# Kernel tuning notes

Hardware: AMD Instinct MI355X
Metric: run time of the kernel (lower is better)

Reference implementation:

```python
import jax, jax.numpy as jnp
import numpy as np

N_NODES = 100000
N_EDGES = 1600000
IN_DIM = 128
HID = 128
OUT = 128
NUM_GRAPHS = 2048


def setup_inputs() -> dict:
    key = jax.random.key(0)
    ks = jax.random.split(key, 10)
    x = jax.random.normal(ks[0], (N_NODES, IN_DIM), dtype=jnp.float32)
    edge_index = jax.random.randint(ks[1], (2, N_EDGES), 0, N_NODES, dtype=jnp.int32)
    graph_index = jnp.sort(jax.random.randint(ks[2], (N_NODES,), 0, NUM_GRAPHS, dtype=jnp.int32))
    def glorot(k, fi, fo):
        lim = jnp.sqrt(6.0 / (fi + fo)).astype(jnp.float32)
        return jax.random.uniform(k, (fi, fo), jnp.float32, -lim, lim)
    return {
        "x": x,
        "edge_index": edge_index,
        "graph_index": graph_index,
        "num_graphs": NUM_GRAPHS,
        "W1": glorot(ks[3], IN_DIM, HID), "b1": jnp.zeros((HID,), jnp.float32),
        "W2": glorot(ks[4], HID, HID),    "b2": jnp.zeros((HID,), jnp.float32),
        "W3": glorot(ks[5], HID, OUT),    "b3": jnp.zeros((OUT,), jnp.float32),
    }


def _gcn_layer(x, src, dst, norm, W, b, n_nodes):
    # transform first (cheap GEMM), then normalized gather-scatter aggregation
    h = x @ W                              # [N, F]
    msg = h[src] * norm[:, None]           # [E+N, F] gather + scale
    out = jax.ops.segment_sum(msg, dst, num_segments=n_nodes)  # scatter-add
    return out + b


def reference(x, edge_index, graph_index, num_graphs, W1, b1, W2, b2, W3, b3):
    n = x.shape[0]
    # add self-loops (PyG GCNConv default)
    loops = jnp.arange(n, dtype=edge_index.dtype)
    src = jnp.concatenate([edge_index[0], loops])
    dst = jnp.concatenate([edge_index[1], loops])
    # symmetric normalization D^-1/2 (A+I) D^-1/2, degree = in-degree incl. self-loop
    deg = jax.ops.segment_sum(jnp.ones_like(src, dtype=x.dtype), dst, num_segments=n)
    dinv = jax.lax.rsqrt(jnp.maximum(deg, 1.0))
    norm = dinv[src] * dinv[dst]
    # 3 conv layers + ReLU (dropout = identity at inference)
    h = jax.nn.relu(_gcn_layer(x, src, dst, norm, W1, b1, n))
    h = jax.nn.relu(_gcn_layer(h, src, dst, norm, W2, b2, n))
    h = jax.nn.relu(_gcn_layer(h, src, dst, norm, W3, b3, n))
    # global mean / max pooling per graph
    gsum = jax.ops.segment_sum(h, graph_index, num_segments=num_graphs)
    cnt = jax.ops.segment_sum(jnp.ones((n,), h.dtype), graph_index, num_segments=num_graphs)
    gmean = gsum / jnp.maximum(cnt, 1.0)[:, None]
    gmax = jax.ops.segment_max(h, graph_index, num_segments=num_graphs)
    return jnp.concatenate([gmean, gmax], axis=-1)
```

## Files before the change

kernel.cpp:

```cpp
#include <hip/hip_runtime.h>
#include <hip/hip_bf16.h>
#include <stdint.h>

#define N_NODES   100000
#define N_EDGES   1600000
#define FDIM      128
#define NUM_GR    2048
#define CSR_CAP   64

#define NBKT      391
#define BKT_CAP   4864
#define TILE      2048
#define LBIN_CAP  24

typedef __attribute__((ext_vector_type(8))) short short8;
typedef __attribute__((ext_vector_type(4))) float f32x4;

__device__ __forceinline__ uint32_t pk2(float a, float b) {
    __hip_bfloat16 x = __float2bfloat16(a), y = __float2bfloat16(b);
    uint16_t ux = *reinterpret_cast<uint16_t*>(&x);
    uint16_t uy = *reinterpret_cast<uint16_t*>(&y);
    return (uint32_t)ux | ((uint32_t)uy << 16);
}

__device__ __forceinline__ float bflo(uint32_t u) { return __uint_as_float(u << 16); }
__device__ __forceinline__ float bfhi(uint32_t u) { return __uint_as_float(u & 0xFFFF0000u); }


__global__ __launch_bounds__(256) void k_bucket_wprep(
        const int* __restrict__ src, const int* __restrict__ dst,
        int* __restrict__ bkt_cnt, int* __restrict__ bkt, int E, int gA,
        const float* __restrict__ W1, const float* __restrict__ W2,
        const float* __restrict__ W3, __hip_bfloat16* __restrict__ wt) {
    int b = blockIdx.x;
    if (b >= gA) {
        int idx = (b - gA) * 256 + threadIdx.x;
        int l = idx >> 14, rem = idx & 16383, c = rem >> 7, k = rem & 127;
        const float* W = (l == 0) ? W1 : ((l == 1) ? W2 : W3);
        wt[idx] = __float2bfloat16(W[k * FDIM + c]);
        return;
    }

    __shared__ int binCnt[NBKT];
    __shared__ int binBase[NBKT];
    __shared__ int bins[NBKT * LBIN_CAP];

    for (int i = threadIdx.x; i < NBKT; i += 256) binCnt[i] = 0;
    __syncthreads();

    int e0 = b * TILE;
    int e1 = min(E, e0 + TILE);
    for (int e = e0 + threadIdx.x; e < e1; e += 256) {
        int s = src[e];
        int d = dst[e];
        int bi = d >> 8;
        int rec = ((d & 255) << 17) | s;
        int pos = atomicAdd(&binCnt[bi], 1);
        if (pos < LBIN_CAP) {
            bins[bi * LBIN_CAP + pos] = rec;
        } else {
            int gp = atomicAdd(&bkt_cnt[bi], 1);
            if (gp < BKT_CAP) bkt[bi * BKT_CAP + gp] = rec;
        }
    }
    __syncthreads();

    for (int i = threadIdx.x; i < NBKT; i += 256) {
        int c = min(binCnt[i], LBIN_CAP);
        binBase[i] = (c > 0) ? atomicAdd(&bkt_cnt[i], c) : 0;
    }
    __syncthreads();

    for (int i = threadIdx.x; i < NBKT * LBIN_CAP; i += 256) {
        int bi = i / LBIN_CAP, sl = i - bi * LBIN_CAP;
        if (sl < min(binCnt[bi], LBIN_CAP)) {
            int gp = binBase[bi] + sl;
            if (gp < BKT_CAP) bkt[bi * BKT_CAP + gp] = bins[i];
        }
    }
}


__global__ __launch_bounds__(256) void k_csr(const int* __restrict__ bkt_cnt,
                                             const int* __restrict__ bkt,
                                             int* __restrict__ cnt,
                                             float* __restrict__ dinv,
                                             int* __restrict__ csr, int n) {
    __shared__ int lc[256];
    __shared__ int cur[256];
    int b = blockIdx.x;
    int tid = threadIdx.x;
    lc[tid] = 0;
    cur[tid] = 0;
    __syncthreads();

    int len = min(bkt_cnt[b], BKT_CAP);
    const int* recs = bkt + b * BKT_CAP;

    for (int i = tid; i < len; i += 256)
        atomicAdd(&lc[(recs[i] >> 17) & 255], 1);
    __syncthreads();

    int v = (b << 8) + tid;
    if (v < n) {
        int c = lc[tid];
        cnt[v] = c;
        dinv[v] = rsqrtf((float)(c + 1));
    }

    for (int i = tid; i < len; i += 256) {
        int rec = recs[i];
        int dl = (rec >> 17) & 255;
        int pos = atomicAdd(&cur[dl], 1);
        if (pos < CSR_CAP)
            csr[(((size_t)(b << 8) + dl) << 6) + pos] = rec & 0x1FFFF;
    }
}


template<bool AF32>
__global__ __launch_bounds__(256) void k_gemm(const void* __restrict__ Ap,
                                              const __hip_bfloat16* __restrict__ Wt,
                                              const float* __restrict__ dinv,
                                              __hip_bfloat16* __restrict__ C, int n) {
    __shared__ uint32_t lds[2 * 128 * 64];
    uint32_t* Atl = lds;
    uint32_t* Wtl = lds + 128 * 64;

    const int tid = threadIdx.x;
    const int rowBase = blockIdx.x * 128;

    if constexpr (AF32) {
        const float* A = (const float*)Ap;
        for (int it = 0; it < 16; ++it) {
            int g = it * 256 + tid;
            int r = g >> 5;
            int seg = g & 31;
            float4 v = make_float4(0.f, 0.f, 0.f, 0.f);
            if (rowBase + r < n) v = *(const float4*)&A[(size_t)(rowBase + r) * FDIM + seg * 4];
            int gg = seg >> 1;
            int word = r * 64 + (((gg ^ (r & 7)) << 2) | ((seg & 1) << 1));
            uint2 pv;
            pv.x = pk2(v.x, v.y);
            pv.y = pk2(v.z, v.w);
            *(uint2*)&Atl[word] = pv;
        }
    } else {
        const uint4* A4 = (const uint4*)Ap;
        for (int it = 0; it < 8; ++it) {
            int g = it * 256 + tid;
            int r = g >> 4;
            int seg = g & 15;
            uint4 v = make_uint4(0, 0, 0, 0);
            if (rowBase + r < n) v = A4[((size_t)rowBase + r) * 16 + seg];
            int word = r * 64 + ((seg ^ (r & 7)) << 2);
            *(uint4*)&Atl[word] = v;
        }
    }
    for (int it = 0; it < 8; ++it) {
        int g = it * 256 + tid;
        int r = g >> 4;
        int seg = g & 15;
        uint4 v = *(const uint4*)&Wt[(size_t)r * FDIM + seg * 8];
        int word = r * 64 + ((seg ^ (r & 7)) << 2);
        *(uint4*)&Wtl[word] = v;
    }
    __syncthreads();

    const int w = tid >> 6;
    const int lane = tid & 63;
    const int r = lane & 15;
    const int q = lane >> 4;

    f32x4 acc[8][2] = {};

#pragma unroll
    for (int kk = 0; kk < 4; ++kk) {
        int gr = ((kk * 4 + q) ^ (r & 7)) << 2;
        short8 a0 = *(const short8*)&Atl[(w * 32 + r) * 64 + gr];
        short8 a1 = *(const short8*)&Atl[(w * 32 + 16 + r) * 64 + gr];
#pragma unroll
        for (int m = 0; m < 8; ++m) {
            short8 bw = *(const short8*)&Wtl[(m * 16 + r) * 64 + gr];
            acc[m][0] = __builtin_amdgcn_mfma_f32_16x16x32_bf16(bw, a0, acc[m][0], 0, 0, 0);
            acc[m][1] = __builtin_amdgcn_mfma_f32_16x16x32_bf16(bw, a1, acc[m][1], 0, 0, 0);
        }
    }

#pragma unroll
    for (int nt = 0; nt < 2; ++nt) {
        int node = rowBase + w * 32 + nt * 16 + r;
        if (node < n) {
            float dv = dinv[node];
#pragma unroll
            for (int m = 0; m < 8; ++m) {
                f32x4 v = acc[m][nt];
                uint2 pv;
                pv.x = pk2(v[0] * dv, v[1] * dv);
                pv.y = pk2(v[2] * dv, v[3] * dv);
                *(uint2*)&C[(size_t)node * FDIM + m * 16 + q * 4] = pv;
            }
        }
    }
}


template<int OUTF>
__global__ __launch_bounds__(256) void k_agg(const __hip_bfloat16* __restrict__ T,
                                             const int* __restrict__ cnt,
                                             const int* __restrict__ csr,
                                             const float* __restrict__ dinv,
                                             const float* __restrict__ bias,
                                             uint32_t* __restrict__ Hb,
                                             float* __restrict__ Hf,
                                             int n) {
    int wid = (blockIdx.x * 256 + threadIdx.x) >> 6;
    int lane = threadIdx.x & 63;
    if (wid >= n) return;
    int v = wid;
    int half = lane >> 5;
    int sub  = lane & 31;

    const uint2* Tu2 = (const uint2*)T;

    uint2 su = Tu2[(size_t)v * 32 + sub];
    float a0, a1, a2, a3;
    if (half == 0) { a0 = bflo(su.x); a1 = bfhi(su.x); a2 = bflo(su.y); a3 = bfhi(su.y); }
    else           { a0 = a1 = a2 = a3 = 0.f; }

    int cv = min(cnt[v], CSR_CAP);

    int sidx = 0;
    if (lane < cv) sidx = csr[((size_t)v << 6) + lane];

    int mr = (cv + 15) & ~15;
    for (int j = 0; j < mr; j += 16) {
        uint2 gg[8]; float ww[8];
#pragma unroll
        for (int t = 0; t < 8; ++t) {
            int el = j + 2 * t + half;
            int it = __shfl(sidx, el, 64);
            ww[t]  = (el < cv) ? 1.f : 0.f;
            gg[t]  = Tu2[(size_t)it * 32 + sub];
        }
#pragma unroll
        for (int t = 0; t < 8; ++t) {
            a0 = fmaf(ww[t], bflo(gg[t].x), a0);
            a1 = fmaf(ww[t], bfhi(gg[t].x), a1);
            a2 = fmaf(ww[t], bflo(gg[t].y), a2);
            a3 = fmaf(ww[t], bfhi(gg[t].y), a3);
        }
    }

    float p0 = __shfl(a0, lane ^ 32, 64);
    float p1 = __shfl(a1, lane ^ 32, 64);
    float p2 = __shfl(a2, lane ^ 32, 64);
    float p3 = __shfl(a3, lane ^ 32, 64);
    a0 += p0; a1 += p1; a2 += p2; a3 += p3;

    if (half == 0) {
        float dv = dinv[v];
        float4 bb = *(const float4*)&bias[sub * 4];
        a0 = fmaxf(fmaf(dv, a0, bb.x), 0.f);
        a1 = fmaxf(fmaf(dv, a1, bb.y), 0.f);
        a2 = fmaxf(fmaf(dv, a2, bb.z), 0.f);
        a3 = fmaxf(fmaf(dv, a3, bb.w), 0.f);
        if constexpr (OUTF == 0) {
            uint2 pv;
            pv.x = pk2(a0, a1);
            pv.y = pk2(a2, a3);
            *(uint2*)&Hb[(size_t)v * 64 + sub * 2] = pv;
        } else {
            *(float4*)&Hf[(size_t)v * FDIM + sub * 4] = make_float4(a0, a1, a2, a3);
        }
    }
}


__global__ __launch_bounds__(256) void k_pool(const float* __restrict__ H,
                                              const int* __restrict__ gidx,
                                              float* __restrict__ gsum,
                                              float* __restrict__ gmax, int n) {
    int wid = (blockIdx.x * 256 + threadIdx.x) >> 6;
    int lane = threadIdx.x & 63;
    int v0 = wid * 64;
    if (v0 >= n) return;
    int v1 = min(n, v0 + 64);

    int cur = gidx[v0];
    float s0 = 0.f, s1 = 0.f, m0 = 0.f, m1 = 0.f;

    for (int v = v0; v < v1; ++v) {
        int g = gidx[v];
        if (g != cur) {
            atomicAdd(&gsum[(size_t)cur * FDIM + lane * 2], s0);
            atomicAdd(&gsum[(size_t)cur * FDIM + lane * 2 + 1], s1);
            atomicMax((unsigned int*)&gmax[(size_t)cur * FDIM + lane * 2], __float_as_uint(m0));
            atomicMax((unsigned int*)&gmax[(size_t)cur * FDIM + lane * 2 + 1], __float_as_uint(m1));
            s0 = s1 = m0 = m1 = 0.f;
            cur = g;
        }
        float2 hv = *(const float2*)&H[(size_t)v * FDIM + lane * 2];
        s0 += hv.x; s1 += hv.y;
        m0 = fmaxf(m0, hv.x); m1 = fmaxf(m1, hv.y);
    }
    atomicAdd(&gsum[(size_t)cur * FDIM + lane * 2], s0);
    atomicAdd(&gsum[(size_t)cur * FDIM + lane * 2 + 1], s1);
    atomicMax((unsigned int*)&gmax[(size_t)cur * FDIM + lane * 2], __float_as_uint(m0));
    atomicMax((unsigned int*)&gmax[(size_t)cur * FDIM + lane * 2 + 1], __float_as_uint(m1));
}

__device__ __forceinline__ int lower_bound_dev(const int* a, int n, int key) {
    int lo = 0, hi = n;
    while (lo < hi) {
        int m = (lo + hi) >> 1;
        if (a[m] < key) lo = m + 1; else hi = m;
    }
    return lo;
}

__global__ void k_finalize(const float* __restrict__ gsum, const float* __restrict__ gmax,
                           const int* __restrict__ gidx, int n, float* __restrict__ out) {
    int idx = blockIdx.x * 256 + threadIdx.x;
    if (idx >= NUM_GR * FDIM) return;
    int g = idx >> 7;
    int f = idx & 127;
    int lo = lower_bound_dev(gidx, n, g);
    int hi = lower_bound_dev(gidx, n, g + 1);
    int c = hi - lo;
    float mean = gsum[(size_t)g * FDIM + f] / (float)max(c, 1);
    out[(size_t)g * 2 * FDIM + f] = mean;
    out[(size_t)g * 2 * FDIM + FDIM + f] = gmax[(size_t)g * FDIM + f];
}


extern "C" void kernel_launch(void* const* d_in, const int* in_sizes, int n_in,
                              void* d_out, int out_size, void* d_ws, size_t ws_size,
                              hipStream_t stream) {
    const float* x    = (const float*)d_in[0];
    const int*   ei   = (const int*)d_in[1];
    const int*   gidx = (const int*)d_in[2];
    const float* W1 = (const float*)d_in[4];
    const float* b1 = (const float*)d_in[5];
    const float* W2 = (const float*)d_in[6];
    const float* b2 = (const float*)d_in[7];
    const float* W3 = (const float*)d_in[8];
    const float* b3 = (const float*)d_in[9];
    float* out = (float*)d_out;

    const int N = N_NODES, E = N_EDGES;
    const int* src = ei;
    const int* dst = ei + E;

    char* ws = (char*)d_ws;
    size_t o = 0;
    auto alloc = [&](size_t bytes) { size_t r = o; o += (bytes + 255) & ~(size_t)255; return r; };
    size_t o_bktcnt = alloc((size_t)NBKT * 4);
    size_t o_bkt    = alloc((size_t)NBKT * BKT_CAP * 4);
    size_t o_cnt    = alloc((size_t)N * 4);
    size_t o_dinv   = alloc((size_t)N * 4);
    size_t o_csr    = alloc((size_t)NBKT * 256 * CSR_CAP * 4);
    size_t o_wt     = alloc((size_t)3 * FDIM * FDIM * 2);
    size_t o_t      = alloc((size_t)N * FDIM * 2);
    size_t o_h      = alloc((size_t)N * FDIM * 4);
    size_t o_gsum   = alloc((size_t)NUM_GR * FDIM * 4);
    size_t o_gmax   = alloc((size_t)NUM_GR * FDIM * 4);

    int*   bkt_cnt = (int*)(ws + o_bktcnt);
    int*   bkt     = (int*)(ws + o_bkt);
    int*   cnt     = (int*)(ws + o_cnt);
    float* dinv    = (float*)(ws + o_dinv);
    int*   csr     = (int*)(ws + o_csr);
    __hip_bfloat16* wtbuf = (__hip_bfloat16*)(ws + o_wt);
    __hip_bfloat16* tbuf  = (__hip_bfloat16*)(ws + o_t);
    __hip_bfloat16* hb16  = (__hip_bfloat16*)(ws + o_h);
    float* hf32    = (float*)(ws + o_h);
    float* gsum    = (float*)(ws + o_gsum);
    float* gmax    = (float*)(ws + o_gmax);

    hipMemsetAsync(bkt_cnt, 0, (size_t)NBKT * 4, stream);
    hipMemsetAsync(gsum, 0, (size_t)NUM_GR * FDIM * 4 * 2, stream);

    const int gA = (E + TILE - 1) / TILE;

    k_bucket_wprep<<<gA + 192, 256, 0, stream>>>(src, dst, bkt_cnt, bkt, E, gA,
                                                 W1, W2, W3, wtbuf);
    k_csr<<<NBKT, 256, 0, stream>>>(bkt_cnt, bkt, cnt, dinv, csr, N);

    const int gGemm = (N + 127) / 128;
    const int gAgg  = (N + 3) / 4;

    k_gemm<true><<<gGemm, 256, 0, stream>>>(x, wtbuf, dinv, tbuf, N);
    k_agg<0><<<gAgg, 256, 0, stream>>>(tbuf, cnt, csr, dinv, b1,
                                       (uint32_t*)hb16, nullptr, N);
    k_gemm<false><<<gGemm, 256, 0, stream>>>(hb16, wtbuf + FDIM * FDIM, dinv, tbuf, N);
    k_agg<0><<<gAgg, 256, 0, stream>>>(tbuf, cnt, csr, dinv, b2,
                                       (uint32_t*)hb16, nullptr, N);
    k_gemm<false><<<gGemm, 256, 0, stream>>>(hb16, wtbuf + 2 * FDIM * FDIM, dinv, tbuf, N);
    k_agg<1><<<gAgg, 256, 0, stream>>>(tbuf, cnt, csr, dinv, b3,
                                       nullptr, hf32, N);

    const int nWaves = (N + 63) / 64;
    const int gPool = (nWaves + 3) / 4;
    k_pool<<<gPool, 256, 0, stream>>>(hf32, gidx, gsum, gmax, N);
    k_finalize<<<(NUM_GR * FDIM + 255) / 256, 256, 0, stream>>>(gsum, gmax, gidx, N, out);
}
```

Baseline: 449.0 us.

## Overlap first-layer GEMM with edge bucketing by folding degree scaling into aggregation

The layer-1 GEMM no longer needs dinv, so it now runs in the same launch as edge bucketing and weight prep, with block ranges selecting the role and shared memory unioned. To make that possible, the first aggregation applies per-edge weights dinv[src]*dinv[dst] and a dinv^2 self weight, fetched through shuffles. Neighbor gathers switch to nontemporal loads, and the bucketing flush becomes a serial per-bin loop. This removes one serialized launch and lets the GEMM hide the atomic-heavy bucketing, at the cost of extra dinv gathers in layer-1 aggregation and shared-memory sizing set by the larger GEMM role.

```diff
diff --git a/kernel.cpp b/kernel.cpp
--- a/kernel.cpp
+++ b/kernel.cpp
@@ -23,59 +23,143 @@
     return (uint32_t)ux | ((uint32_t)uy << 16);
 }
 
+__device__ __forceinline__ unsigned short bf16h(float f) {
+    __hip_bfloat16 h = __float2bfloat16(f);
+    return *reinterpret_cast<unsigned short*>(&h);
+}
+
 __device__ __forceinline__ float bflo(uint32_t u) { return __uint_as_float(u << 16); }
 __device__ __forceinline__ float bfhi(uint32_t u) { return __uint_as_float(u & 0xFFFF0000u); }
 
-
-__global__ __launch_bounds__(256) void k_bucket_wprep(
+__device__ __forceinline__ uint2 ntload2(const uint2* p) {
+    unsigned long long r = __builtin_nontemporal_load((const unsigned long long*)p);
+    uint2 o; o.x = (unsigned)r; o.y = (unsigned)(r >> 32);
+    return o;
+}
+
+
+union SmemA {
+    uint32_t gemm[2 * 128 * 64];
+    struct { int binCnt[NBKT]; int bins[NBKT * LBIN_CAP]; } bk;
+};
+
+__global__ __launch_bounds__(256) void k_mega(
         const int* __restrict__ src, const int* __restrict__ dst,
-        int* __restrict__ bkt_cnt, int* __restrict__ bkt, int E, int gA,
-        const float* __restrict__ W1, const float* __restrict__ W2,
-        const float* __restrict__ W3, __hip_bfloat16* __restrict__ wt) {
-    int b = blockIdx.x;
-    if (b >= gA) {
-        int idx = (b - gA) * 256 + threadIdx.x;
+        int* __restrict__ bkt_cnt, int* __restrict__ bkt, int E, int gBkt,
+        const float* __restrict__ x, const float* __restrict__ W1,
+        __hip_bfloat16* __restrict__ C, int n, int gGemm,
+        const float* __restrict__ W2, const float* __restrict__ W3,
+        __hip_bfloat16* __restrict__ wt) {
+    __shared__ SmemA smem;
+    const int b = blockIdx.x;
+    const int tid = threadIdx.x;
+
+    if (b < gBkt) {
+        for (int i = tid; i < NBKT; i += 256) smem.bk.binCnt[i] = 0;
+        __syncthreads();
+
+        int e0 = b * TILE;
+        int e1 = min(E, e0 + TILE);
+        for (int e = e0 + tid; e < e1; e += 256) {
+            int s = src[e];
+            int d = dst[e];
+            int bi = d >> 8;
+            int rec = ((d & 255) << 17) | s;
+            int pos = atomicAdd(&smem.bk.binCnt[bi], 1);
+            if (pos < LBIN_CAP) {
+                smem.bk.bins[bi * LBIN_CAP + pos] = rec;
+            } else {
+                int gp = atomicAdd(&bkt_cnt[bi], 1);
+                if (gp < BKT_CAP) bkt[bi * BKT_CAP + gp] = rec;
+            }
+        }
+        __syncthreads();
+
+        for (int i = tid; i < NBKT; i += 256) {
+            int c = min(smem.bk.binCnt[i], LBIN_CAP);
+            if (c > 0) {
+                int base = atomicAdd(&bkt_cnt[i], c);
+                for (int j = 0; j < c; ++j) {
+                    int gp = base + j;
+                    if (gp < BKT_CAP) bkt[i * BKT_CAP + gp] = smem.bk.bins[i * LBIN_CAP + j];
+                }
+            }
+        }
+        return;
+    }
+
+    if (b >= gBkt + gGemm) {
+        int idx = (b - gBkt - gGemm) * 256 + tid;
         int l = idx >> 14, rem = idx & 16383, c = rem >> 7, k = rem & 127;
-        const float* W = (l == 0) ? W1 : ((l == 1) ? W2 : W3);
+        const float* W = (l == 0) ? W2 : W3;
         wt[idx] = __float2bfloat16(W[k * FDIM + c]);
         return;
     }
 
-    __shared__ int binCnt[NBKT];
-    __shared__ int binBase[NBKT];
-    __shared__ int bins[NBKT * LBIN_CAP];
-
-    for (int i = threadIdx.x; i < NBKT; i += 256) binCnt[i] = 0;
+    uint32_t* Atl = smem.gemm;
+    uint32_t* Wtl = smem.gemm + 128 * 64;
+    const int rowBase = (b - gBkt) * 128;
+
+    for (int it = 0; it < 16; ++it) {
+        int g = it * 256 + tid;
+        int r = g >> 5;
+        int seg = g & 31;
+        float4 v = make_float4(0.f, 0.f, 0.f, 0.f);
+        if (rowBase + r < n) v = *(const float4*)&x[(size_t)(rowBase + r) * FDIM + seg * 4];
+        int gg = seg >> 1;
+        int word = r * 64 + (((gg ^ (r & 7)) << 2) | ((seg & 1) << 1));
+        uint2 pv;
+        pv.x = pk2(v.x, v.y);
+        pv.y = pk2(v.z, v.w);
+        *(uint2*)&Atl[word] = pv;
+    }
+    for (int it = 0; it < 16; ++it) {
+        int g = it * 256 + tid;
+        int k = g >> 5;
+        int cs = g & 31;
+        float4 wv = *(const float4*)&W1[k * FDIM + cs * 4];
+        float vals[4] = {wv.x, wv.y, wv.z, wv.w};
+#pragma unroll
+        for (int j = 0; j < 4; ++j) {
+            int c = cs * 4 + j;
+            int aw = c * 64 + (((k >> 3) ^ (c & 7)) << 2) + ((k >> 1) & 3);
+            ((unsigned short*)Wtl)[aw * 2 + (k & 1)] = bf16h(vals[j]);
+        }
+    }
     __syncthreads();
 
-    int e0 = b * TILE;
-    int e1 = min(E, e0 + TILE);
-    for (int e = e0 + threadIdx.x; e < e1; e += 256) {
-        int s = src[e];
-        int d = dst[e];
-        int bi = d >> 8;
-        int rec = ((d & 255) << 17) | s;
-        int pos = atomicAdd(&binCnt[bi], 1);
-        if (pos < LBIN_CAP) {
-            bins[bi * LBIN_CAP + pos] = rec;
-        } else {
-            int gp = atomicAdd(&bkt_cnt[bi], 1);
-            if (gp < BKT_CAP) bkt[bi * BKT_CAP + gp] = rec;
-        }
-    }
-    __syncthreads();
-
-    for (int i = threadIdx.x; i < NBKT; i += 256) {
-        int c = min(binCnt[i], LBIN_CAP);
-        binBase[i] = (c > 0) ? atomicAdd(&bkt_cnt[i], c) : 0;
-    }
-    __syncthreads();
-
-    for (int i = threadIdx.x; i < NBKT * LBIN_CAP; i += 256) {
-        int bi = i / LBIN_CAP, sl = i - bi * LBIN_CAP;
-        if (sl < min(binCnt[bi], LBIN_CAP)) {
-            int gp = binBase[bi] + sl;
-            if (gp < BKT_CAP) bkt[bi * BKT_CAP + gp] = bins[i];
+    const int w = tid >> 6;
+    const int lane = tid & 63;
+    const int r = lane & 15;
+    const int q = lane >> 4;
+
+    f32x4 acc[8][2] = {};
+
+#pragma unroll
+    for (int kk = 0; kk < 4; ++kk) {
+        int gr = ((kk * 4 + q) ^ (r & 7)) << 2;
+        short8 a0 = *(const short8*)&Atl[(w * 32 + r) * 64 + gr];
+        short8 a1 = *(const short8*)&Atl[(w * 32 + 16 + r) * 64 + gr];
+#pragma unroll
+        for (int m = 0; m < 8; ++m) {
+            short8 bw = *(const short8*)&Wtl[(m * 16 + r) * 64 + gr];
+            acc[m][0] = __builtin_amdgcn_mfma_f32_16x16x32_bf16(bw, a0, acc[m][0], 0, 0, 0);
+            acc[m][1] = __builtin_amdgcn_mfma_f32_16x16x32_bf16(bw, a1, acc[m][1], 0, 0, 0);
+        }
+    }
+
+#pragma unroll
+    for (int nt = 0; nt < 2; ++nt) {
+        int node = rowBase + w * 32 + nt * 16 + r;
+        if (node < n) {
+#pragma unroll
+            for (int m = 0; m < 8; ++m) {
+                f32x4 v = acc[m][nt];
+                uint2 pv;
+                pv.x = pk2(v[0], v[1]);
+                pv.y = pk2(v[2], v[3]);
+                *(uint2*)&C[(size_t)node * FDIM + m * 16 + q * 4] = pv;
+            }
         }
     }
 }
@@ -118,8 +202,7 @@
 }
 
 
-template<bool AF32>
-__global__ __launch_bounds__(256) void k_gemm(const void* __restrict__ Ap,
+__global__ __launch_bounds__(256) void k_gemm(const __hip_bfloat16* __restrict__ Ap,
                                               const __hip_bfloat16* __restrict__ Wt,
                                               const float* __restrict__ dinv,
                                               __hip_bfloat16* __restrict__ C, int n) {
@@ -130,32 +213,15 @@
     const int tid = threadIdx.x;
     const int rowBase = blockIdx.x * 128;
 
-    if constexpr (AF32) {
-        const float* A = (const float*)Ap;
-        for (int it = 0; it < 16; ++it) {
-            int g = it * 256 + tid;
-            int r = g >> 5;
-            int seg = g & 31;
-            float4 v = make_float4(0.f, 0.f, 0.f, 0.f);
-            if (rowBase + r < n) v = *(const float4*)&A[(size_t)(rowBase + r) * FDIM + seg * 4];
-            int gg = seg >> 1;
-            int word = r * 64 + (((gg ^ (r & 7)) << 2) | ((seg & 1) << 1));
-            uint2 pv;
-            pv.x = pk2(v.x, v.y);
-            pv.y = pk2(v.z, v.w);
-            *(uint2*)&Atl[word] = pv;
-        }
-    } else {
-        const uint4* A4 = (const uint4*)Ap;
-        for (int it = 0; it < 8; ++it) {
-            int g = it * 256 + tid;
-            int r = g >> 4;
-            int seg = g & 15;
-            uint4 v = make_uint4(0, 0, 0, 0);
-            if (rowBase + r < n) v = A4[((size_t)rowBase + r) * 16 + seg];
-            int word = r * 64 + ((seg ^ (r & 7)) << 2);
-            *(uint4*)&Atl[word] = v;
-        }
+    const uint4* A4 = (const uint4*)Ap;
+    for (int it = 0; it < 8; ++it) {
+        int g = it * 256 + tid;
+        int r = g >> 4;
+        int seg = g & 15;
+        uint4 v = make_uint4(0, 0, 0, 0);
+        if (rowBase + r < n) v = A4[((size_t)rowBase + r) * 16 + seg];
+        int word = r * 64 + ((seg ^ (r & 7)) << 2);
+        *(uint4*)&Atl[word] = v;
     }
     for (int it = 0; it < 8; ++it) {
         int g = it * 256 + tid;
@@ -205,7 +271,7 @@
 }
 
 
-template<int OUTF>
+template<int OUTF, int WEIGHTED>
 __global__ __launch_bounds__(256) void k_agg(const __hip_bfloat16* __restrict__ T,
                                              const int* __restrict__ cnt,
                                              const int* __restrict__ csr,
@@ -223,15 +289,26 @@
 
     const uint2* Tu2 = (const uint2*)T;
 
+    float dv = dinv[v];
+
     uint2 su = Tu2[(size_t)v * 32 + sub];
     float a0, a1, a2, a3;
-    if (half == 0) { a0 = bflo(su.x); a1 = bfhi(su.x); a2 = bflo(su.y); a3 = bfhi(su.y); }
-    else           { a0 = a1 = a2 = a3 = 0.f; }
+    if (half == 0) {
+        float ws = WEIGHTED ? dv * dv : 1.f;
+        a0 = ws * bflo(su.x); a1 = ws * bfhi(su.x);
+        a2 = ws * bflo(su.y); a3 = ws * bfhi(su.y);
+    } else {
+        a0 = a1 = a2 = a3 = 0.f;
+    }
 
     int cv = min(cnt[v], CSR_CAP);
 
-    int sidx = 0;
-    if (lane < cv) sidx = csr[((size_t)v << 6) + lane];
+    int   sidx = 0;
+    float wv   = 0.f;
+    if (lane < cv) {
+        sidx = csr[((size_t)v << 6) + lane];
+        if (WEIGHTED) wv = dinv[sidx] * dv;
+    }
 
     int mr = (cv + 15) & ~15;
     for (int j = 0; j < mr; j += 16) {
@@ -240,8 +317,9 @@
         for (int t = 0; t < 8; ++t) {
             int el = j + 2 * t + half;
             int it = __shfl(sidx, el, 64);
-            ww[t]  = (el < cv) ? 1.f : 0.f;
-            gg[t]  = Tu2[(size_t)it * 32 + sub];
+            if (WEIGHTED) ww[t] = __shfl(wv, el, 64);
+            else          ww[t] = (el < cv) ? 1.f : 0.f;
+            gg[t] = ntload2(&Tu2[(size_t)it * 32 + sub]);
         }
 #pragma unroll
         for (int t = 0; t < 8; ++t) {
@@ -259,12 +337,18 @@
     a0 += p0; a1 += p1; a2 += p2; a3 += p3;
 
     if (half == 0) {
-        float dv = dinv[v];
         float4 bb = *(const float4*)&bias[sub * 4];
-        a0 = fmaxf(fmaf(dv, a0, bb.x), 0.f);
-        a1 = fmaxf(fmaf(dv, a1, bb.y), 0.f);
-        a2 = fmaxf(fmaf(dv, a2, bb.z), 0.f);
-        a3 = fmaxf(fmaf(dv, a3, bb.w), 0.f);
+        if (WEIGHTED) {
+            a0 = fmaxf(a0 + bb.x, 0.f);
+            a1 = fmaxf(a1 + bb.y, 0.f);
+            a2 = fmaxf(a2 + bb.z, 0.f);
+            a3 = fmaxf(a3 + bb.w, 0.f);
+        } else {
+            a0 = fmaxf(fmaf(dv, a0, bb.x), 0.f);
+            a1 = fmaxf(fmaf(dv, a1, bb.y), 0.f);
+            a2 = fmaxf(fmaf(dv, a2, bb.z), 0.f);
+            a3 = fmaxf(fmaf(dv, a3, bb.w), 0.f);
+        }
         if constexpr (OUTF == 0) {
             uint2 pv;
             pv.x = pk2(a0, a1);
@@ -360,7 +444,7 @@
     size_t o_cnt    = alloc((size_t)N * 4);
     size_t o_dinv   = alloc((size_t)N * 4);
     size_t o_csr    = alloc((size_t)NBKT * 256 * CSR_CAP * 4);
-    size_t o_wt     = alloc((size_t)3 * FDIM * FDIM * 2);
+    size_t o_wt     = alloc((size_t)2 * FDIM * FDIM * 2);
     size_t o_t      = alloc((size_t)N * FDIM * 2);
     size_t o_h      = alloc((size_t)N * FDIM * 4);
     size_t o_gsum   = alloc((size_t)NUM_GR * FDIM * 4);
@@ -381,24 +465,23 @@
     hipMemsetAsync(bkt_cnt, 0, (size_t)NBKT * 4, stream);
     hipMemsetAsync(gsum, 0, (size_t)NUM_GR * FDIM * 4 * 2, stream);
 
-    const int gA = (E + TILE - 1) / TILE;
-
-    k_bucket_wprep<<<gA + 192, 256, 0, stream>>>(src, dst, bkt_cnt, bkt, E, gA,
-                                                 W1, W2, W3, wtbuf);
-    k_csr<<<NBKT, 256, 0, stream>>>(bkt_cnt, bkt, cnt, dinv, csr, N);
-
+    const int gBkt  = (E + TILE - 1) / TILE;
     const int gGemm = (N + 127) / 128;
     const int gAgg  = (N + 3) / 4;
 
-    k_gemm<true><<<gGemm, 256, 0, stream>>>(x, wtbuf, dinv, tbuf, N);
-    k_agg<0><<<gAgg, 256, 0, stream>>>(tbuf, cnt, csr, dinv, b1,
-                                       (uint32_t*)hb16, nullptr, N);
-    k_gemm<false><<<gGemm, 256, 0, stream>>>(hb16, wtbuf + FDIM * FDIM, dinv, tbuf, N);
-    k_agg<0><<<gAgg, 256, 0, stream>>>(tbuf, cnt, csr, dinv, b2,
-                                       (uint32_t*)hb16, nullptr, N);
-    k_gemm<false><<<gGemm, 256, 0, stream>>>(hb16, wtbuf + 2 * FDIM * FDIM, dinv, tbuf, N);
-    k_agg<1><<<gAgg, 256, 0, stream>>>(tbuf, cnt, csr, dinv, b3,
-                                       nullptr, hf32, N);
+    k_mega<<<gBkt + gGemm + 128, 256, 0, stream>>>(src, dst, bkt_cnt, bkt, E, gBkt,
+                                                   x, W1, tbuf, N, gGemm,
+                                                   W2, W3, wtbuf);
+    k_csr<<<NBKT, 256, 0, stream>>>(bkt_cnt, bkt, cnt, dinv, csr, N);
+
+    k_agg<0, 1><<<gAgg, 256, 0, stream>>>(tbuf, cnt, csr, dinv, b1,
+                                          (uint32_t*)hb16, nullptr, N);
+    k_gemm<<<gGemm, 256, 0, stream>>>(hb16, wtbuf, dinv, tbuf, N);
+    k_agg<0, 0><<<gAgg, 256, 0, stream>>>(tbuf, cnt, csr, dinv, b2,
+                                          (uint32_t*)hb16, nullptr, N);
+    k_gemm<<<gGemm, 256, 0, stream>>>(hb16, wtbuf + FDIM * FDIM, dinv, tbuf, N);
+    k_agg<1, 0><<<gAgg, 256, 0, stream>>>(tbuf, cnt, csr, dinv, b3,
+                                          nullptr, hf32, N);
 
     const int nWaves = (N + 63) / 64;
     const int gPool = (nWaves + 3) / 4;
```

After: 548.9 us. 22.3% more time.
